# Performance work log

Measured on AMD Instinct MI355X. Metric: run time of the kernel, lower is better.

Reference implementation:

```python
import jax, jax.numpy as jnp
import numpy as np

B, S, D, H = 2, 2048, 1024, 16
HD = D // H  # head dim = 64

def setup_inputs() -> dict:
    key = jax.random.key(0)
    ks = jax.random.split(key, 11)
    s = 0.02
    return {
        "query": jax.random.normal(ks[0], (B, S, D), jnp.float32),
        "key_in": jax.random.normal(ks[1], (B, S, D), jnp.float32),
        "value": jax.random.normal(ks[2], (B, S, D), jnp.float32),
        "Wq": jax.random.normal(ks[3], (D, D), jnp.float32) * s,
        "bq": jnp.zeros((D,), jnp.float32),
        "Wk": jax.random.normal(ks[4], (D, D), jnp.float32) * s,
        "bk": jnp.zeros((D,), jnp.float32),
        "Wv": jax.random.normal(ks[5], (D, D), jnp.float32) * s,
        "bv": jnp.zeros((D,), jnp.float32),
        "Wo": jax.random.normal(ks[6], (D, D), jnp.float32) * s,
        "bo": jnp.zeros((D,), jnp.float32),
    }

def _split_heads(x):
    b, s, _ = x.shape
    return x.reshape(b, s, H, HD).transpose(0, 2, 1, 3)  # [B,H,S,HD]

def reference(query, key_in, value, Wq, bq, Wk, bk, Wv, bv, Wo, bo):
    q = _split_heads(query @ Wq + bq)
    k = _split_heads(key_in @ Wk + bk)
    v = _split_heads(value @ Wv + bv)
    scores = jnp.einsum("bhqd,bhkd->bhqk", q, k) / jnp.sqrt(jnp.float32(HD))
    weights = jax.nn.softmax(scores, axis=-1)  # dropout = identity (eval)
    ctx = jnp.einsum("bhqk,bhkd->bhqd", weights, v)
    ctx = ctx.transpose(0, 2, 1, 3).reshape(query.shape[0], -1, D)
    return ctx @ Wo + bo
```

## Files before the change

### kernel.cpp

```cpp
#include <hip/hip_runtime.h>
#include <hip/hip_bf16.h>


typedef __attribute__((ext_vector_type(8))) short short8;
typedef __attribute__((ext_vector_type(4))) short short4v;
typedef __attribute__((ext_vector_type(4))) float f32x4;

static __device__ __forceinline__ short f2bf(float f) {
    union { float f; unsigned u; } c; c.f = f;
    unsigned r = c.u + 0x7fff + ((c.u >> 16) & 1);
    return (short)(r >> 16);
}

static __device__ __forceinline__ unsigned pk_bf16(float a, float b) {
    union { __hip_bfloat162 h; unsigned u; } c;
    c.h = __float22bfloat162_rn(make_float2(a, b));
    return c.u;
}

typedef const void __attribute__((address_space(1)))* gas_ptr;
typedef void __attribute__((address_space(3)))* las_ptr;
static __device__ __forceinline__ void gload16(const void* g, void* l) {
    __builtin_amdgcn_global_load_lds((gas_ptr)g, (las_ptr)l, 16, 0, 0);
}

__global__ __launch_bounds__(256) void prep(
    const float* __restrict__ X0, const float* __restrict__ X1,
    const float* __restrict__ X2, short* __restrict__ Abf,
    const float* __restrict__ W0, const float* __restrict__ W1,
    const float* __restrict__ W2, const float* __restrict__ W3,
    short* __restrict__ Wt)
{
    __shared__ float tile[32][33];
    const int bid = blockIdx.x;
    if (bid < 6144) {
        const int zz = bid >> 11, xb = bid & 2047;
        const float* X = zz == 0 ? X0 : zz == 1 ? X1 : X2;
        short* o = Abf + ((size_t)zz << 22);
        const int i = (xb * 256 + threadIdx.x) * 8;
        const float4 a = *(const float4*)(X + i);
        const float4 b = *(const float4*)(X + i + 4);
        uint4 r;
        r.x = pk_bf16(a.x, a.y); r.y = pk_bf16(a.z, a.w);
        r.z = pk_bf16(b.x, b.y); r.w = pk_bf16(b.z, b.w);
        *(uint4*)(o + i) = r;
    } else {
        const int wid = bid - 6144;
        const int z = wid >> 10;
        const float* W = z == 0 ? W0 : z == 1 ? W1 : z == 2 ? W2 : W3;
        short* O = Wt + ((size_t)z << 20);
        const int k0 = (wid & 31) * 32, n0 = ((wid >> 5) & 31) * 32;
        const int tx = threadIdx.x & 31, ty = threadIdx.x >> 5;
        #pragma unroll
        for (int j = 0; j < 32; j += 8)
            tile[ty + j][tx] = W[(k0 + ty + j) * 1024 + n0 + tx];
        __syncthreads();
        #pragma unroll
        for (int j = 0; j < 32; j += 8)
            O[(n0 + ty + j) * 1024 + k0 + tx] = f2bf(tile[tx][ty + j]);
    }
}

#define STAGE(buf, k0) do {                                                   \
    gload16(Aa + (size_t)(gm0 + (t >> 2)) * 1024 + (k0) + (t & 3) * 8,        \
            &Al[buf][w * 512]);                                               \
    _Pragma("unroll")                                                         \
    for (int j = 0; j < 2; ++j) {                                             \
        const int c = j * 256 + t;                                            \
        gload16(Ba + (size_t)(gn0 + (c >> 2)) * 1024 + (k0) + (c & 3) * 8,    \
                &Bl[buf][j * 2048 + w * 512]);                                \
    }                                                                         \
} while (0)

#define GEMM_CORE(Aa_, Ba_, m0v, n0v)                                         \
    __shared__ short Al[2][2048];                           \
    __shared__ short Bl[2][4096];                          \
    const int t = threadIdx.x;                                                \
    const int gm0 = (m0v), gn0 = (n0v);                                       \
    const int lane = t & 63, w = t >> 6;                                      \
    const int lm = lane & 15, lg = lane >> 4;                                 \
    const int wr = w >> 1, wc = w & 1;                                        \
    f32x4 acc[2][4] = {};                                                     \
    STAGE(0, 0);                                                              \
    __syncthreads();                                                          \
    int buf = 0;                                                              \
    for (int kk = 0; kk < 32; ++kk) {                                         \
        if (kk < 31) STAGE(buf ^ 1, (kk + 1) * 32);                           \
        const short* Ab = Al[buf];                                            \
        const short* Bb = Bl[buf];                                            \
        short8 af[2], bfr[4];                                                 \
        _Pragma("unroll")                                                     \
        for (int mf = 0; mf < 2; ++mf)                                        \
            af[mf] = *(const short8*)(Ab + (wr * 32 + mf * 16 + lm) * 32 + lg * 8); \
        _Pragma("unroll")                                                     \
        for (int nf = 0; nf < 4; ++nf)                                        \
            bfr[nf] = *(const short8*)(Bb + (wc * 64 + nf * 16 + lm) * 32 + lg * 8); \
        _Pragma("unroll")                                                     \
        for (int mf = 0; mf < 2; ++mf)                                        \
            _Pragma("unroll")                                                 \
            for (int nf = 0; nf < 4; ++nf)                                    \
                acc[mf][nf] = __builtin_amdgcn_mfma_f32_16x16x32_bf16(        \
                    af[mf], bfr[nf], acc[mf][nf], 0, 0, 0);                   \
        __syncthreads();                                                      \
        buf ^= 1;                                                             \
    }

__global__ __launch_bounds__(256) void gemmqkv(
    const short* __restrict__ Abase, const short* __restrict__ Wt,
    const float* __restrict__ bq, const float* __restrict__ bk,
    const float* __restrict__ bv, short* __restrict__ Qh,
    short* __restrict__ Kh, short* __restrict__ Vt, float qscale)
{
    const int flat = blockIdx.z * 512 + blockIdx.y * 8 + blockIdx.x;
    const int remap = (flat & 7) * 192 + (flat >> 3);
    const int z = remap >> 9;
    const int rem = remap & 511;
    const int m0 = (rem >> 3) * 64, n0 = (rem & 7) * 128;

    const short* Aa = Abase + ((size_t)z << 22);
    const short* Ba = Wt + ((size_t)z << 20);
    const float* bias = z == 0 ? bq : z == 1 ? bk : bv;
    short* O = z == 0 ? Qh : z == 1 ? Kh : Vt;
    const float scale = z == 0 ? qscale : 1.0f;

    GEMM_CORE(Aa, Ba, m0, n0)

    #pragma unroll
    for (int mf = 0; mf < 2; ++mf) {
        const int mb = m0 + wr * 32 + mf * 16 + lg * 4;
        #pragma unroll
        for (int nf = 0; nf < 4; ++nf) {
            const int n = n0 + wc * 64 + nf * 16 + lm;
            const float bs = bias[n];
            if (z == 2) {
                short4v sv;
                #pragma unroll
                for (int i = 0; i < 4; ++i)
                    sv[i] = f2bf(acc[mf][nf][i] + bs);
                const int addr = (((mb >> 11) * 16 + (n >> 6)) * 64 + (n & 63)) * 2048 + (mb & 2047);
                *(short4v*)&O[addr] = sv;
            } else {
                #pragma unroll
                for (int i = 0; i < 4; ++i) {
                    const int m = mb + i;
                    const int addr = (((m >> 11) * 16 + (n >> 6)) * 2048 + (m & 2047)) * 64 + (n & 63);
                    O[addr] = f2bf(scale * (acc[mf][nf][i] + bs));
                }
            }
        }
    }
}

__global__ __launch_bounds__(256) void gemmo(
    const short* __restrict__ Aa, const short* __restrict__ Ba,
    const float* __restrict__ bias, float* __restrict__ Out)
{
    const int flat = blockIdx.y * 8 + blockIdx.x;
    const int remap = (flat & 7) * 64 + (flat >> 3);
    const int m0 = (remap >> 3) * 64, n0 = (remap & 7) * 128;

    GEMM_CORE(Aa, Ba, m0, n0)

    #pragma unroll
    for (int mf = 0; mf < 2; ++mf) {
        const int mb = m0 + wr * 32 + mf * 16 + lg * 4;
        #pragma unroll
        for (int nf = 0; nf < 4; ++nf) {
            const int n = n0 + wc * 64 + nf * 16 + lm;
            const float bs = bias[n];
            #pragma unroll
            for (int i = 0; i < 4; ++i)
                Out[(mb + i) * 1024 + n] = acc[mf][nf][i] + bs;
        }
    }
}
#undef STAGE
#undef GEMM_CORE

__global__ __launch_bounds__(512, 4) void attn_k(
    const short* __restrict__ Q, const short* __restrict__ K,
    const short* __restrict__ V, short* __restrict__ Ctx)
{
    __shared__ short Kl[2][128][64];
    __shared__ short Vl[2][2][64][64];
    __shared__ short Pl[8][16][64];
    const int t = threadIdx.x;
    const int qt = blockIdx.x, bh = blockIdx.y;
    const int lane = t & 63, w = t >> 6;
    const int lm = lane & 15, lg = lane >> 4;
    const int swz = (lm & 7) << 3;
    const int swc = lm & 7;

    const int qrow = qt * 128 + w * 16 + lm;
    short8 qf[2];
    #pragma unroll
    for (int ks = 0; ks < 2; ++ks)
        qf[ks] = *(const short8*)(Q + ((size_t)bh * 2048 + qrow) * 64 + ks * 32 + lg * 8);

    float m_run = -3e38f, l_run = 0.f;
    f32x4 o_acc[4] = {};

    const int rk = t >> 2, ck = t & 3;
    const int rv = t >> 3, cv = t & 7;
    const short* Kg = K + ((size_t)bh * 2048 + rk) * 64 + ck * 16;
    const short* Vg = V + ((size_t)bh * 64 + rv) * 2048 + cv * 16;
    const int koff0 = rk * 64 + ((ck * 2) ^ (rk & 7)) * 8;
    const int koff1 = rk * 64 + ((ck * 2 + 1) ^ (rk & 7)) * 8;
    const int vhalf = (cv >> 2) * 4096;
    const int voff0 = vhalf + rv * 64 + (((cv * 2) & 7) ^ (rv & 7)) * 8;
    const int voff1 = vhalf + rv * 64 + (((cv * 2 + 1) & 7) ^ (rv & 7)) * 8;

    {
        short8 a = *(const short8*)(Kg);
        short8 b = *(const short8*)(Kg + 8);
        short8 c = *(const short8*)(Vg);
        short8 d = *(const short8*)(Vg + 8);
        *(short8*)((short*)Kl[0] + koff0) = a;
        *(short8*)((short*)Kl[0] + koff1) = b;
        *(short8*)((short*)Vl[0] + voff0) = c;
        *(short8*)((short*)Vl[0] + voff1) = d;
    }

    short* prow = &Pl[w][lm][0];
    int cur = 0;

    for (int kt = 0; kt < 16; ++kt) {
        __syncthreads();

        short8 kn0, kn1, vn0, vn1;
        const bool pfn = (kt < 15);
        if (pfn) {
            const short* Kgn = Kg + (size_t)(kt + 1) * 8192;
            const short* Vgn = Vg + (kt + 1) * 128;
            kn0 = *(const short8*)(Kgn);
            kn1 = *(const short8*)(Kgn + 8);
            vn0 = *(const short8*)(Vgn);
            vn1 = *(const short8*)(Vgn + 8);
        }

        const short* Kc = (const short*)Kl[cur];
        const short* Vc = (const short*)Vl[cur];

        f32x4 sa[2][4] = {};
        #pragma unroll
        for (int h = 0; h < 2; ++h)
            #pragma unroll
            for (int nf = 0; nf < 4; ++nf) {
                const int rr = h * 64 + nf * 16 + lm;
                #pragma unroll
                for (int ks = 0; ks < 2; ++ks) {
                    const short8 kf = *(const short8*)(Kc + rr * 64 + ((ks * 4 + lg) ^ swc) * 8);
                    sa[h][nf] = __builtin_amdgcn_mfma_f32_16x16x32_bf16(kf, qf[ks], sa[h][nf], 0, 0, 0);
                }
            }

        float mx[8];
        #pragma unroll
        for (int h = 0; h < 2; ++h)
            #pragma unroll
            for (int nf = 0; nf < 4; ++nf) {
                const f32x4 v = sa[h][nf];
                mx[h * 4 + nf] = fmaxf(fmaxf(v[0], v[1]), fmaxf(v[2], v[3]));
            }
        float mt = fmaxf(fmaxf(fmaxf(mx[0], mx[1]), fmaxf(mx[2], mx[3])),
                         fmaxf(fmaxf(mx[4], mx[5]), fmaxf(mx[6], mx[7])));
        mt = fmaxf(mt, __shfl_xor(mt, 16));
        mt = fmaxf(mt, __shfl_xor(mt, 32));
        if (__any(mt > m_run + 8.0f)) {
            const float mn = fmaxf(m_run, mt);
            const float alpha = exp2f(m_run - mn);
            l_run *= alpha;
            #pragma unroll
            for (int nf = 0; nf < 4; ++nf)
                #pragma unroll
                for (int i = 0; i < 4; ++i)
                    o_acc[nf][i] *= alpha;
            m_run = mn;
        }
        float ps[8];
        #pragma unroll
        for (int h = 0; h < 2; ++h)
            #pragma unroll
            for (int nf = 0; nf < 4; ++nf) {
                f32x4 v = sa[h][nf];
                #pragma unroll
                for (int i = 0; i < 4; ++i) v[i] = exp2f(v[i] - m_run);
                sa[h][nf] = v;
                ps[h * 4 + nf] = (v[0] + v[1]) + (v[2] + v[3]);
            }
        float rs = ((ps[0] + ps[1]) + (ps[2] + ps[3])) +
                   ((ps[4] + ps[5]) + (ps[6] + ps[7]));
        rs += __shfl_xor(rs, 16);
        rs += __shfl_xor(rs, 32);
        l_run += rs;

        #pragma unroll
        for (int h = 0; h < 2; ++h) {
            #pragma unroll
            for (int nf = 0; nf < 4; ++nf) {
                uint2 pv;
                pv.x = pk_bf16(sa[h][nf][0], sa[h][nf][1]);
                pv.y = pk_bf16(sa[h][nf][2], sa[h][nf][3]);
                *(uint2*)(prow + ((nf * 16 + lg * 4) ^ swz)) = pv;
            }
            short8 pf[2];
            #pragma unroll
            for (int ks = 0; ks < 2; ++ks)
                pf[ks] = *(const short8*)(prow + ((ks * 32 + lg * 8) ^ swz));

            if (h == 0 && pfn) {
                short* Kn = (short*)Kl[cur ^ 1];
                short* Vn = (short*)Vl[cur ^ 1];
                *(short8*)(Kn + koff0) = kn0;
                *(short8*)(Kn + koff1) = kn1;
                *(short8*)(Vn + voff0) = vn0;
                *(short8*)(Vn + voff1) = vn1;
            }

            #pragma unroll
            for (int nf = 0; nf < 4; ++nf) {
                const int rr = nf * 16 + lm;
                #pragma unroll
                for (int ks = 0; ks < 2; ++ks) {
                    const short8 vf = *(const short8*)(Vc + h * 4096 + rr * 64 + ((ks * 4 + lg) ^ swc) * 8);
                    o_acc[nf] = __builtin_amdgcn_mfma_f32_16x16x32_bf16(vf, pf[ks], o_acc[nf], 0, 0, 0);
                }
            }
        }
        cur ^= 1;
    }

    const float inv = 1.f / l_run;
    const int b = bh >> 4, h = bh & 15;
    short* outp = Ctx + ((size_t)b * 2048 + qrow) * 1024 + h * 64 + lg * 4;
    #pragma unroll
    for (int nf = 0; nf < 4; ++nf) {
        uint2 pk;
        pk.x = pk_bf16(o_acc[nf][0] * inv, o_acc[nf][1] * inv);
        pk.y = pk_bf16(o_acc[nf][2] * inv, o_acc[nf][3] * inv);
        *(uint2*)(outp + nf * 16) = pk;
    }
}

extern "C" void kernel_launch(void* const* d_in, const int* in_sizes, int n_in,
                              void* d_out, int out_size, void* d_ws, size_t ws_size,
                              hipStream_t stream)
{
    const float* query  = (const float*)d_in[0];
    const float* key_in = (const float*)d_in[1];
    const float* value  = (const float*)d_in[2];
    const float* Wq = (const float*)d_in[3];
    const float* bq = (const float*)d_in[4];
    const float* Wk = (const float*)d_in[5];
    const float* bk = (const float*)d_in[6];
    const float* Wv = (const float*)d_in[7];
    const float* bv = (const float*)d_in[8];
    const float* Wo = (const float*)d_in[9];
    const float* bo = (const float*)d_in[10];
    float* out = (float*)d_out;

    char* ws = (char*)d_ws;
    short* Wt  = (short*)(ws);
    short* Abf = (short*)(ws + (8  << 20));
    short* Qh  = (short*)(ws + (32 << 20));
    short* Kh  = (short*)(ws + (40 << 20));
    short* Vt  = (short*)(ws + (48 << 20));
    short* Ctx = Abf;

    const float qscale = 0.125f * 1.44269504088896f;

    hipLaunchKernelGGL(prep, dim3(10240), dim3(256), 0, stream,
                       query, key_in, value, Abf, Wq, Wk, Wv, Wo, Wt);
    hipLaunchKernelGGL(gemmqkv, dim3(8, 64, 3), dim3(256), 0, stream,
                       Abf, Wt, bq, bk, bv, Qh, Kh, Vt, qscale);
    hipLaunchKernelGGL(attn_k, dim3(16, 32), dim3(512), 0, stream,
                       Qh, Kh, Vt, Ctx);
    hipLaunchKernelGGL(gemmo, dim3(8, 64), dim3(256), 0, stream,
                       Ctx, Wt + (3 << 20), bo, out);
}
```

Baseline: 155.0 us.

## Rewrite attention kernel with 32x32x16 MFMA, 4 waves of 32 query rows

The flash-attention kernel moves from 16x16x32 bf16 MFMA with 8 waves of 16 query rows each to 32x32x16 MFMA with 4 waves of 32 rows each. The K/V tile per iteration shrinks from 128 to 64 keys, doubling the loop trip count. The P staging buffer is restructured to match. The larger MFMA shape is meant to raise operand reuse per LDS read and cut cross-lane shuffles in the softmax reductions. In exchange it uses more accumulator registers per lane, lowers the occupancy hint, and adds more barriers per block.

```diff
diff --git a/kernel.cpp b/kernel.cpp
--- a/kernel.cpp
+++ b/kernel.cpp
@@ -5,6 +5,7 @@
 typedef __attribute__((ext_vector_type(8))) short short8;
 typedef __attribute__((ext_vector_type(4))) short short4v;
 typedef __attribute__((ext_vector_type(4))) float f32x4;
+typedef __attribute__((ext_vector_type(16))) float f32x16;
 
 static __device__ __forceinline__ short f2bf(float f) {
     union { float f; unsigned u; } c; c.f = f;
@@ -177,38 +178,33 @@
 #undef STAGE
 #undef GEMM_CORE
 
-__global__ __launch_bounds__(512, 4) void attn_k(
+__global__ __launch_bounds__(256, 3) void attn_k(
     const short* __restrict__ Q, const short* __restrict__ K,
     const short* __restrict__ V, short* __restrict__ Ctx)
 {
-    __shared__ short Kl[2][128][64];
-    __shared__ short Vl[2][2][64][64];
-    __shared__ short Pl[8][16][64];
+    __shared__ short Kl[2][64][64];
+    __shared__ short Vl[2][64][64];
+    __shared__ short Pl[4][32][40];
     const int t = threadIdx.x;
     const int qt = blockIdx.x, bh = blockIdx.y;
     const int lane = t & 63, w = t >> 6;
-    const int lm = lane & 15, lg = lane >> 4;
-    const int swz = (lm & 7) << 3;
-    const int swc = lm & 7;
-
-    const int qrow = qt * 128 + w * 16 + lm;
-    short8 qf[2];
+    const int lq = lane & 31, hi = lane >> 5;
+    const int swc = lq & 7;
+
+    const int qrow = qt * 128 + w * 32 + lq;
+    short8 qf[4];
     #pragma unroll
-    for (int ks = 0; ks < 2; ++ks)
-        qf[ks] = *(const short8*)(Q + ((size_t)bh * 2048 + qrow) * 64 + ks * 32 + lg * 8);
+    for (int dc = 0; dc < 4; ++dc)
+        qf[dc] = *(const short8*)(Q + ((size_t)bh * 2048 + qrow) * 64 + dc * 16 + hi * 8);
 
     float m_run = -3e38f, l_run = 0.f;
-    f32x4 o_acc[4] = {};
+    f32x16 o_acc[2] = {};
 
     const int rk = t >> 2, ck = t & 3;
-    const int rv = t >> 3, cv = t & 7;
     const short* Kg = K + ((size_t)bh * 2048 + rk) * 64 + ck * 16;
-    const short* Vg = V + ((size_t)bh * 64 + rv) * 2048 + cv * 16;
+    const short* Vg = V + ((size_t)bh * 64 + rk) * 2048 + ck * 16;
     const int koff0 = rk * 64 + ((ck * 2) ^ (rk & 7)) * 8;
     const int koff1 = rk * 64 + ((ck * 2 + 1) ^ (rk & 7)) * 8;
-    const int vhalf = (cv >> 2) * 4096;
-    const int voff0 = vhalf + rv * 64 + (((cv * 2) & 7) ^ (rv & 7)) * 8;
-    const int voff1 = vhalf + rv * 64 + (((cv * 2 + 1) & 7) ^ (rv & 7)) * 8;
 
     {
         short8 a = *(const short8*)(Kg);
@@ -217,21 +213,21 @@
         short8 d = *(const short8*)(Vg + 8);
         *(short8*)((short*)Kl[0] + koff0) = a;
         *(short8*)((short*)Kl[0] + koff1) = b;
-        *(short8*)((short*)Vl[0] + voff0) = c;
-        *(short8*)((short*)Vl[0] + voff1) = d;
-    }
-
-    short* prow = &Pl[w][lm][0];
+        *(short8*)((short*)Vl[0] + koff0) = c;
+        *(short8*)((short*)Vl[0] + koff1) = d;
+    }
+
+    short* prow = &Pl[w][lq][0];
     int cur = 0;
 
-    for (int kt = 0; kt < 16; ++kt) {
+    for (int kt = 0; kt < 32; ++kt) {
         __syncthreads();
 
         short8 kn0, kn1, vn0, vn1;
-        const bool pfn = (kt < 15);
+        const bool pfn = (kt < 31);
         if (pfn) {
-            const short* Kgn = Kg + (size_t)(kt + 1) * 8192;
-            const short* Vgn = Vg + (kt + 1) * 128;
+            const short* Kgn = Kg + (size_t)(kt + 1) * 4096;
+            const short* Vgn = Vg + (kt + 1) * 64;
             kn0 = *(const short8*)(Kgn);
             kn1 = *(const short8*)(Kgn + 8);
             vn0 = *(const short8*)(Vgn);
@@ -241,105 +237,101 @@
         const short* Kc = (const short*)Kl[cur];
         const short* Vc = (const short*)Vl[cur];
 
-        f32x4 sa[2][4] = {};
-        #pragma unroll
-        for (int h = 0; h < 2; ++h)
-            #pragma unroll
-            for (int nf = 0; nf < 4; ++nf) {
-                const int rr = h * 64 + nf * 16 + lm;
-                #pragma unroll
-                for (int ks = 0; ks < 2; ++ks) {
-                    const short8 kf = *(const short8*)(Kc + rr * 64 + ((ks * 4 + lg) ^ swc) * 8);
-                    sa[h][nf] = __builtin_amdgcn_mfma_f32_16x16x32_bf16(kf, qf[ks], sa[h][nf], 0, 0, 0);
-                }
-            }
-
-        float mx[8];
-        #pragma unroll
-        for (int h = 0; h < 2; ++h)
-            #pragma unroll
-            for (int nf = 0; nf < 4; ++nf) {
-                const f32x4 v = sa[h][nf];
-                mx[h * 4 + nf] = fmaxf(fmaxf(v[0], v[1]), fmaxf(v[2], v[3]));
-            }
-        float mt = fmaxf(fmaxf(fmaxf(mx[0], mx[1]), fmaxf(mx[2], mx[3])),
-                         fmaxf(fmaxf(mx[4], mx[5]), fmaxf(mx[6], mx[7])));
-        mt = fmaxf(mt, __shfl_xor(mt, 16));
+        f32x16 sacc[2] = {};
+        #pragma unroll
+        for (int kb = 0; kb < 2; ++kb) {
+            const int krow = kb * 32 + lq;
+            #pragma unroll
+            for (int dc = 0; dc < 4; ++dc) {
+                const short8 kf = *(const short8*)(Kc + krow * 64 + ((dc * 2 + hi) ^ swc) * 8);
+                sacc[kb] = __builtin_amdgcn_mfma_f32_32x32x16_bf16(kf, qf[dc], sacc[kb], 0, 0, 0);
+            }
+        }
+
+        float m8[8];
+        #pragma unroll
+        for (int kb = 0; kb < 2; ++kb)
+            #pragma unroll
+            for (int g = 0; g < 4; ++g)
+                m8[kb * 4 + g] = fmaxf(fmaxf(sacc[kb][g * 4 + 0], sacc[kb][g * 4 + 1]),
+                                       fmaxf(sacc[kb][g * 4 + 2], sacc[kb][g * 4 + 3]));
+        float mt = fmaxf(fmaxf(fmaxf(m8[0], m8[1]), fmaxf(m8[2], m8[3])),
+                         fmaxf(fmaxf(m8[4], m8[5]), fmaxf(m8[6], m8[7])));
         mt = fmaxf(mt, __shfl_xor(mt, 32));
         if (__any(mt > m_run + 8.0f)) {
             const float mn = fmaxf(m_run, mt);
             const float alpha = exp2f(m_run - mn);
             l_run *= alpha;
             #pragma unroll
-            for (int nf = 0; nf < 4; ++nf)
+            for (int db = 0; db < 2; ++db)
                 #pragma unroll
-                for (int i = 0; i < 4; ++i)
-                    o_acc[nf][i] *= alpha;
+                for (int r = 0; r < 16; ++r)
+                    o_acc[db][r] *= alpha;
             m_run = mn;
         }
         float ps[8];
         #pragma unroll
-        for (int h = 0; h < 2; ++h)
-            #pragma unroll
-            for (int nf = 0; nf < 4; ++nf) {
-                f32x4 v = sa[h][nf];
-                #pragma unroll
-                for (int i = 0; i < 4; ++i) v[i] = exp2f(v[i] - m_run);
-                sa[h][nf] = v;
-                ps[h * 4 + nf] = (v[0] + v[1]) + (v[2] + v[3]);
+        for (int kb = 0; kb < 2; ++kb)
+            #pragma unroll
+            for (int g = 0; g < 4; ++g) {
+                float e0 = exp2f(sacc[kb][g * 4 + 0] - m_run);
+                float e1 = exp2f(sacc[kb][g * 4 + 1] - m_run);
+                float e2 = exp2f(sacc[kb][g * 4 + 2] - m_run);
+                float e3 = exp2f(sacc[kb][g * 4 + 3] - m_run);
+                sacc[kb][g * 4 + 0] = e0; sacc[kb][g * 4 + 1] = e1;
+                sacc[kb][g * 4 + 2] = e2; sacc[kb][g * 4 + 3] = e3;
+                ps[kb * 4 + g] = (e0 + e1) + (e2 + e3);
             }
         float rs = ((ps[0] + ps[1]) + (ps[2] + ps[3])) +
                    ((ps[4] + ps[5]) + (ps[6] + ps[7]));
-        rs += __shfl_xor(rs, 16);
         rs += __shfl_xor(rs, 32);
         l_run += rs;
 
         #pragma unroll
-        for (int h = 0; h < 2; ++h) {
-            #pragma unroll
-            for (int nf = 0; nf < 4; ++nf) {
-                uint2 pv;
-                pv.x = pk_bf16(sa[h][nf][0], sa[h][nf][1]);
-                pv.y = pk_bf16(sa[h][nf][2], sa[h][nf][3]);
-                *(uint2*)(prow + ((nf * 16 + lg * 4) ^ swz)) = pv;
-            }
-            short8 pf[2];
-            #pragma unroll
-            for (int ks = 0; ks < 2; ++ks)
-                pf[ks] = *(const short8*)(prow + ((ks * 32 + lg * 8) ^ swz));
-
-            if (h == 0 && pfn) {
+        for (int kb = 0; kb < 2; ++kb) {
+            #pragma unroll
+            for (int g = 0; g < 4; ++g) {
+                uint2 pv2;
+                pv2.x = pk_bf16(sacc[kb][g * 4 + 0], sacc[kb][g * 4 + 1]);
+                pv2.y = pk_bf16(sacc[kb][g * 4 + 2], sacc[kb][g * 4 + 3]);
+                *(uint2*)(prow + g * 8 + 4 * hi) = pv2;
+            }
+            const short8 pf0 = *(const short8*)(prow + hi * 8);
+            const short8 pf1 = *(const short8*)(prow + 16 + hi * 8);
+
+            if (kb == 0 && pfn) {
                 short* Kn = (short*)Kl[cur ^ 1];
                 short* Vn = (short*)Vl[cur ^ 1];
                 *(short8*)(Kn + koff0) = kn0;
                 *(short8*)(Kn + koff1) = kn1;
-                *(short8*)(Vn + voff0) = vn0;
-                *(short8*)(Vn + voff1) = vn1;
-            }
-
-            #pragma unroll
-            for (int nf = 0; nf < 4; ++nf) {
-                const int rr = nf * 16 + lm;
-                #pragma unroll
-                for (int ks = 0; ks < 2; ++ks) {
-                    const short8 vf = *(const short8*)(Vc + h * 4096 + rr * 64 + ((ks * 4 + lg) ^ swc) * 8);
-                    o_acc[nf] = __builtin_amdgcn_mfma_f32_16x16x32_bf16(vf, pf[ks], o_acc[nf], 0, 0, 0);
-                }
+                *(short8*)(Vn + koff0) = vn0;
+                *(short8*)(Vn + koff1) = vn1;
+            }
+
+            #pragma unroll
+            for (int db = 0; db < 2; ++db) {
+                const int vrow = db * 32 + lq;
+                const short8 vf0 = *(const short8*)(Vc + vrow * 64 + ((kb * 4 + 0 + hi) ^ swc) * 8);
+                o_acc[db] = __builtin_amdgcn_mfma_f32_32x32x16_bf16(vf0, pf0, o_acc[db], 0, 0, 0);
+                const short8 vf1 = *(const short8*)(Vc + vrow * 64 + ((kb * 4 + 2 + hi) ^ swc) * 8);
+                o_acc[db] = __builtin_amdgcn_mfma_f32_32x32x16_bf16(vf1, pf1, o_acc[db], 0, 0, 0);
             }
         }
         cur ^= 1;
     }
 
     const float inv = 1.f / l_run;
-    const int b = bh >> 4, h = bh & 15;
-    short* outp = Ctx + ((size_t)b * 2048 + qrow) * 1024 + h * 64 + lg * 4;
+    const int b = bh >> 4, hh = bh & 15;
+    short* outp = Ctx + ((size_t)b * 2048 + qrow) * 1024 + hh * 64 + 4 * hi;
     #pragma unroll
-    for (int nf = 0; nf < 4; ++nf) {
-        uint2 pk;
-        pk.x = pk_bf16(o_acc[nf][0] * inv, o_acc[nf][1] * inv);
-        pk.y = pk_bf16(o_acc[nf][2] * inv, o_acc[nf][3] * inv);
-        *(uint2*)(outp + nf * 16) = pk;
-    }
+    for (int db = 0; db < 2; ++db)
+        #pragma unroll
+        for (int g = 0; g < 4; ++g) {
+            uint2 pk2;
+            pk2.x = pk_bf16(o_acc[db][g * 4 + 0] * inv, o_acc[db][g * 4 + 1] * inv);
+            pk2.y = pk_bf16(o_acc[db][g * 4 + 2] * inv, o_acc[db][g * 4 + 3] * inv);
+            *(uint2*)(outp + db * 32 + g * 8) = pk2;
+        }
 }
 
 extern "C" void kernel_launch(void* const* d_in, const int* in_sizes, int n_in,
@@ -373,7 +365,7 @@
                        query, key_in, value, Abf, Wq, Wk, Wv, Wo, Wt);
     hipLaunchKernelGGL(gemmqkv, dim3(8, 64, 3), dim3(256), 0, stream,
                        Abf, Wt, bq, bk, bv, Qh, Kh, Vt, qscale);
-    hipLaunchKernelGGL(attn_k, dim3(16, 32), dim3(512), 0, stream,
+    hipLaunchKernelGGL(attn_k, dim3(16, 32), dim3(256), 0, stream,
                        Qh, Kh, Vt, Ctx);
     hipLaunchKernelGGL(gemmo, dim3(8, 64), dim3(256), 0, stream,
                        Ctx, Wt + (3 << 20), bo, out);
```

Measured after the change: 160.0 us. 1.03x slower.
